# Performance work log

Hardware: AMD Instinct MI355X
Metric: run time of the kernel (lower is better)

Reference implementation:

```python
import jax, jax.numpy as jnp
import numpy as np

B, RULE_DIM, E, P, TOP_K = 8192, 128, 64, 16, 3
EPS = 1e-5
CONF_THRESH = 0.1


def _ln(x, g, b):
    # torch.nn.LayerNorm: biased variance, eps=1e-5
    m = x.mean(-1, keepdims=True)
    v = ((x - m) ** 2).mean(-1, keepdims=True)
    return (x - m) / jnp.sqrt(v + EPS) * g + b


def setup_inputs() -> dict:
    key = jax.random.key(0)
    ks = jax.random.split(key, 8)
    s = lambda fan: 1.0 / np.sqrt(fan)
    return {
        "rule_embedding": jax.random.normal(ks[0], (B, RULE_DIM), jnp.float32),
        "rp_w1": jax.random.normal(ks[1], (RULE_DIM, 256), jnp.float32) * s(RULE_DIM),
        "rp_b1": jnp.zeros((256,), jnp.float32),
        "rp_g1": jnp.ones((256,), jnp.float32),
        "rp_be1": jnp.zeros((256,), jnp.float32),
        "rp_w2": jax.random.normal(ks[2], (256, 512), jnp.float32) * s(256),
        "rp_b2": jnp.zeros((512,), jnp.float32),
        "rp_g2": jnp.ones((512,), jnp.float32),
        "rp_be2": jnp.zeros((512,), jnp.float32),
        "op_w": jax.random.normal(ks[3], (512, E), jnp.float32) * s(512),
        "op_b": jnp.zeros((E,), jnp.float32),
        "pe_w1": jax.random.normal(ks[4], (E, 512, 256), jnp.float32) * s(512),
        "pe_b1": jnp.zeros((E, 256), jnp.float32),
        "pe_g": jnp.ones((E, 256), jnp.float32),
        "pe_beta": jnp.zeros((E, 256), jnp.float32),
        "pe_w2": jax.random.normal(ks[5], (E, 256, P), jnp.float32) * s(256),
        "pe_b2": jnp.zeros((E, P), jnp.float32),
    }


def reference(rule_embedding, rp_w1, rp_b1, rp_g1, rp_be1, rp_w2, rp_b2,
              rp_g2, rp_be2, op_w, op_b, pe_w1, pe_b1, pe_g, pe_beta,
              pe_w2, pe_b2):
    # rule_parser: Linear -> LN -> ReLU -> Linear -> LN -> ReLU
    h = jax.nn.relu(_ln(rule_embedding @ rp_w1 + rp_b1, rp_g1, rp_be1))   # [B,256]
    features = jax.nn.relu(_ln(h @ rp_w2 + rp_b2, rp_g2, rp_be2))         # [B,512]

    # op routing: softmax + top-k
    op_probs = jax.nn.softmax(features @ op_w + op_b, axis=-1)            # [B,E]
    top_probs, top_idx = jax.lax.top_k(op_probs, TOP_K)                   # [B,K]

    # per-op param predictor MLP, evaluated for every expert (vmap over E)
    def expert(w1, b1, g, be, w2, b2):
        z = jax.nn.relu(_ln(features @ w1 + b1, g, be))                   # [B,256]
        return z @ w2 + b2                                                # [B,P]

    h2_all = jax.vmap(expert)(pe_w1, pe_b1, pe_g, pe_beta, pe_w2, pe_b2)  # [E,B,P]

    # gather the selected expert's raw param logits per (token, slot)
    params_sel = h2_all[top_idx, jnp.arange(B)[:, None], :]               # [B,K,P]

    # original skips ops with confidence < 0.1 -> mask them out
    mask = (top_probs >= CONF_THRESH).astype(params_sel.dtype)            # [B,K]
    params_out = params_sel * mask[..., None]

    return top_probs, top_idx, params_out
```

## Files before the change

### kernel.cpp

```cpp
#include <hip/hip_runtime.h>
#include <math.h>

#define Bv   8192
#define EPSv 1e-5f
#define CONFv 0.1f
#define MB (1024*1024)

typedef __attribute__((ext_vector_type(8))) short short8;
typedef __attribute__((ext_vector_type(4))) float f32x4;

__device__ __forceinline__ float wave_sum64(float v){
  #pragma unroll
  for (int o = 32; o; o >>= 1) v += __shfl_xor(v, o, 64);
  return v;
}

__device__ __forceinline__ void split3f(float x, short &h, short &m, short &l){
  unsigned u = __float_as_uint(x);
  h = (short)(u >> 16);
  float r1 = x - __uint_as_float(u & 0xffff0000u);
  unsigned u1 = __float_as_uint(r1);
  m = (short)(u1 >> 16);
  float r2 = r1 - __uint_as_float(u1 & 0xffff0000u);
  l = (short)(__float_as_uint(r2) >> 16);
}

__device__ __forceinline__ void split2f(float x, short &h, short &m){
  unsigned u = __float_as_uint(x);
  h = (short)(u >> 16);
  float r1 = x - __uint_as_float(u & 0xffff0000u);
  m = (short)(__float_as_uint(r1) >> 16);
}

__device__ __forceinline__ f32x4 mfma5(short8 ah, short8 am,
                                       short8 bh, short8 bm, short8 bl, f32x4 c){
  c = __builtin_amdgcn_mfma_f32_16x16x32_bf16(am, bm, c, 0, 0, 0);
  c = __builtin_amdgcn_mfma_f32_16x16x32_bf16(ah, bl, c, 0, 0, 0);
  c = __builtin_amdgcn_mfma_f32_16x16x32_bf16(am, bh, c, 0, 0, 0);
  c = __builtin_amdgcn_mfma_f32_16x16x32_bf16(ah, bm, c, 0, 0, 0);
  c = __builtin_amdgcn_mfma_f32_16x16x32_bf16(ah, bh, c, 0, 0, 0);
  return c;
}

__device__ __forceinline__ f32x4 mfma3(short8 ah, short8 al,
                                       short8 bh, short8 bl, f32x4 c){
  c = __builtin_amdgcn_mfma_f32_16x16x32_bf16(al, bh, c, 0, 0, 0);
  c = __builtin_amdgcn_mfma_f32_16x16x32_bf16(ah, bl, c, 0, 0, 0);
  c = __builtin_amdgcn_mfma_f32_16x16x32_bf16(ah, bh, c, 0, 0, 0);
  return c;
}

__global__ __launch_bounds__(256) void k_pack(const float* __restrict__ pw1,
    const float* __restrict__ pw2, const float* __restrict__ w1,
    const float* __restrict__ w2, const float* __restrict__ opw,
    unsigned short* __restrict__ p1, unsigned short* __restrict__ p2,
    unsigned short* __restrict__ w1p, unsigned short* __restrict__ w2p,
    unsigned short* __restrict__ opwp, int* __restrict__ cnt)
{
  int bid = blockIdx.x;
  if (bid < 4096){
    int t = bid*256 + threadIdx.x;
    int e = t >> 14, rem = t & 16383, kg = rem >> 8, n = rem & 255;
    const float* src = pw1 + ((size_t)e << 17) + (size_t)(kg*8)*256 + n;
    short8 h, l;
    #pragma unroll
    for (int j = 0; j < 8; j++){
      float w = src[(size_t)j*256];
      unsigned u = __float_as_uint(w);
      float r2 = w - __uint_as_float(u & 0xffff0000u);
      h[j] = (short)(u >> 16);
      l[j] = (short)(__float_as_uint(r2) >> 16);
    }
    int idx8 = ((((n >> 4)*16 + (kg >> 2))*64) + (kg & 3)*16 + (n & 15)) << 3;
    unsigned short* ep = p1 + (size_t)e * 262144;
    *(short8*)(ep + idx8)          = h;
    *(short8*)(ep + 131072 + idx8) = l;
  } else if (bid < 4224){
    int t = (bid - 4096)*256 + threadIdx.x;
    int e = t >> 9, rem = t & 511, kg = rem >> 4, n = rem & 15;
    const float* src = pw2 + (size_t)e*4096 + (size_t)(kg*8)*16 + n;
    short8 h, l;
    #pragma unroll
    for (int j = 0; j < 8; j++){
      float w = src[(size_t)j*16];
      unsigned u = __float_as_uint(w);
      float r2 = w - __uint_as_float(u & 0xffff0000u);
      h[j] = (short)(u >> 16);
      l[j] = (short)(__float_as_uint(r2) >> 16);
    }
    int idx8 = (((kg >> 2)*64) + (kg & 3)*16 + n) << 3;
    unsigned short* ep = p2 + (size_t)e * 8192;
    *(short8*)(ep + idx8)        = h;
    *(short8*)(ep + 4096 + idx8) = l;
  } else if (bid < 4352){
    int gid = (bid - 4224)*256 + threadIdx.x;
    int k = gid >> 8, n = gid & 255;
    short h, m, l;
    split3f(w1[gid], h, m, l);
    int idx = (((n >> 4)*4 + (k >> 5))*64 + (((k >> 3) & 3)*16 + (n & 15)))*8 + (k & 7);
    w1p[idx]             = (unsigned short)h;
    w1p[32768 + idx]     = (unsigned short)m;
    w1p[2*32768 + idx]   = (unsigned short)l;
  } else if (bid < 4864){
    int gid = (bid - 4352)*256 + threadIdx.x;
    int k = gid >> 9, n = gid & 511;
    short h, m, l;
    split3f(w2[gid], h, m, l);
    int idx = (((n >> 4)*8 + (k >> 5))*64 + (((k >> 3) & 3)*16 + (n & 15)))*8 + (k & 7);
    w2p[idx]             = (unsigned short)h;
    w2p[131072 + idx]    = (unsigned short)m;
    w2p[2*131072 + idx]  = (unsigned short)l;
  } else if (bid < 4992){
    int gid = (bid - 4864)*256 + threadIdx.x;
    int k = gid >> 6, n = gid & 63;
    short h, m, l;
    split3f(opw[gid], h, m, l);
    int idx = (((n >> 4)*16 + (k >> 5))*64 + (((k >> 3) & 3)*16 + (n & 15)))*8 + (k & 7);
    opwp[idx]            = (unsigned short)h;
    opwp[32768 + idx]    = (unsigned short)m;
    opwp[2*32768 + idx]  = (unsigned short)l;
  } else {
    if (threadIdx.x < 64) cnt[threadIdx.x] = 0;
  }
}

__global__ __launch_bounds__(1024) void k_fused(const float* __restrict__ X,
    const unsigned short* __restrict__ w1p, const float* __restrict__ b1,
    const float* __restrict__ g1, const float* __restrict__ be1,
    const unsigned short* __restrict__ w2p, const float* __restrict__ b2,
    const float* __restrict__ g2, const float* __restrict__ be2,
    const unsigned short* __restrict__ opwp, const float* __restrict__ opb,
    unsigned short* __restrict__ fh, unsigned short* __restrict__ fl,
    float* __restrict__ dout, int* __restrict__ cnt, int* __restrict__ list)
{
  extern __shared__ unsigned char smem[];
  unsigned short* xh  = (unsigned short*)smem;
  unsigned short* xm  = xh + 4096;
  unsigned short* hbh = xh + 8192;
  unsigned short* hbm = xh + 16384;
  unsigned short* gah = xh;
  unsigned short* gam = xh + 16384;
  __shared__ float ps[32][20];
  __shared__ float pq[32][20];
  __shared__ float mi[32][2];
  __shared__ float lg[32][64];

  const int tid = threadIdx.x;
  const int r0  = blockIdx.x * 32;
  const int wave = tid >> 6, lane = tid & 63, lquad = lane >> 4, l15 = lane & 15;

  {
    int r = tid >> 5, c4 = tid & 31;
    float4 v = ((const float4*)X)[(size_t)(r0+r)*32 + c4];
    unsigned u0 = __float_as_uint(v.x), u1 = __float_as_uint(v.y);
    unsigned u2 = __float_as_uint(v.z), u3 = __float_as_uint(v.w);
    float m0 = v.x - __uint_as_float(u0 & 0xffff0000u);
    float m1 = v.y - __uint_as_float(u1 & 0xffff0000u);
    float m2 = v.z - __uint_as_float(u2 & 0xffff0000u);
    float m3 = v.w - __uint_as_float(u3 & 0xffff0000u);
    unsigned hp0 = (u0 >> 16) | (u1 & 0xffff0000u);
    unsigned hp1 = (u2 >> 16) | (u3 & 0xffff0000u);
    unsigned mp0 = (__float_as_uint(m0) >> 16) | (__float_as_uint(m1) & 0xffff0000u);
    unsigned mp1 = (__float_as_uint(m2) >> 16) | (__float_as_uint(m3) & 0xffff0000u);
    int gk = c4 >> 1, half = c4 & 1;
    int off = r*128 + ((gk ^ (r & 7)) << 3) + half*4;
    ((unsigned*)(xh + off))[0] = hp0;
    ((unsigned*)(xh + off))[1] = hp1;
    ((unsigned*)(xm + off))[0] = mp0;
    ((unsigned*)(xm + off))[1] = mp1;
  }
  __syncthreads();

  float bcol1, gcol1, becol1;
  {
    int col = wave*16 + l15;
    bcol1 = b1[col]; gcol1 = g1[col]; becol1 = be1[col];
  }
  {
    f32x4 acc[2];
    acc[0] = (f32x4){0.f,0.f,0.f,0.f};
    acc[1] = (f32x4){0.f,0.f,0.f,0.f};
    const int pstride = 32768;
    for (int ks4 = 0; ks4 < 4; ks4++){
      const unsigned short* bp = w1p + (((wave*4 + ks4)*64 + lane) << 3);
      short8 bh = *(const short8*)bp;
      short8 bm = *(const short8*)(bp + pstride);
      short8 bl = *(const short8*)(bp + 2*pstride);
      #pragma unroll
      for (int mt = 0; mt < 2; mt++){
        int r = mt*16 + l15;
        int off = r*128 + (((ks4*4 + lquad) ^ (r & 7)) << 3);
        short8 ah = *(const short8*)(xh + off);
        short8 am = *(const short8*)(xm + off);
        acc[mt] = mfma5(ah, am, bh, bm, bl, acc[mt]);
      }
    }
    #pragma unroll
    for (int mt = 0; mt < 2; mt++)
      #pragma unroll
      for (int reg = 0; reg < 4; reg++){
        float z = acc[mt][reg] + bcol1;
        float s = z, q = z*z;
        #pragma unroll
        for (int o = 1; o < 16; o <<= 1){ s += __shfl_xor(s, o, 64); q += __shfl_xor(q, o, 64); }
        int row = mt*16 + lquad*4 + reg;
        if (l15 == 0){ ps[row][wave] = s; pq[row][wave] = q; }
      }
    __syncthreads();
    if (tid < 32){
      int row = tid;
      float4 s0 = *(const float4*)&ps[row][0],  s1 = *(const float4*)&ps[row][4];
      float4 s2 = *(const float4*)&ps[row][8],  s3 = *(const float4*)&ps[row][12];
      float4 q0 = *(const float4*)&pq[row][0],  q1 = *(const float4*)&pq[row][4];
      float4 q2 = *(const float4*)&pq[row][8],  q3 = *(const float4*)&pq[row][12];
      float s = s0.x; s += s0.y; s += s0.z; s += s0.w;
      s += s1.x; s += s1.y; s += s1.z; s += s1.w;
      s += s2.x; s += s2.y; s += s2.z; s += s2.w;
      s += s3.x; s += s3.y; s += s3.z; s += s3.w;
      float q = q0.x; q += q0.y; q += q0.z; q += q0.w;
      q += q1.x; q += q1.y; q += q1.z; q += q1.w;
      q += q2.x; q += q2.y; q += q2.z; q += q2.w;
      q += q3.x; q += q3.y; q += q3.z; q += q3.w;
      float mean = s * (1.0f/256.0f);
      float var  = q * (1.0f/256.0f) - mean*mean;
      mi[row][0] = mean;
      mi[row][1] = 1.0f / sqrtf(var + EPSv);
    }
    __syncthreads();
    #pragma unroll
    for (int mt = 0; mt < 2; mt++)
      #pragma unroll
      for (int reg = 0; reg < 4; reg++){
        int row = mt*16 + lquad*4 + reg;
        float2 mv = *(const float2*)mi[row];
        int col = wave*16 + l15;
        float z = acc[mt][reg] + bcol1;
        float y = fmaxf((z - mv.x)*mv.y*gcol1 + becol1, 0.f);
        short hh, mm2;
        split2f(y, hh, mm2);
        int gg = col >> 3, c7 = col & 7;
        int adr = row*256 + ((gg ^ (row & 7)) << 3) + c7;
        hbh[adr] = (unsigned short)hh;
        hbm[adr] = (unsigned short)mm2;
      }
  }
  __syncthreads();

  f32x4 acc2[2][2];
  #pragma unroll
  for (int mt = 0; mt < 2; mt++)
    #pragma unroll
    for (int nt = 0; nt < 2; nt++) acc2[mt][nt] = (f32x4){0.f,0.f,0.f,0.f};
  {
    const int pstride = 131072;
    for (int ks4 = 0; ks4 < 8; ks4++){
      short8 ah[2], am[2];
      #pragma unroll
      for (int mt = 0; mt < 2; mt++){
        int r = mt*16 + l15;
        int off = r*256 + (((ks4*4 + lquad) ^ (r & 7)) << 3);
        ah[mt] = *(const short8*)(hbh + off);
        am[mt] = *(const short8*)(hbm + off);
      }
      #pragma unroll
      for (int nt = 0; nt < 2; nt++){
        int ntg = wave*2 + nt;
        const unsigned short* bp = w2p + (((ntg*8 + ks4)*64 + lane) << 3);
        short8 bh = *(const short8*)bp;
        short8 bm = *(const short8*)(bp + pstride);
        short8 bl = *(const short8*)(bp + 2*pstride);
        #pragma unroll
        for (int mt = 0; mt < 2; mt++)
          acc2[mt][nt] = mfma5(ah[mt], am[mt], bh, bm, bl, acc2[mt][nt]);
      }
    }
  }

  float bcol[2], gcol[2], becol[2];
  #pragma unroll
  for (int nt = 0; nt < 2; nt++){
    int col = (wave*2 + nt)*16 + l15;
    bcol[nt] = b2[col]; gcol[nt] = g2[col]; becol[nt] = be2[col];
  }
  #pragma unroll
  for (int mt = 0; mt < 2; mt++)
    #pragma unroll
    for (int reg = 0; reg < 4; reg++){
      float s = 0.f, q = 0.f;
      #pragma unroll
      for (int nt = 0; nt < 2; nt++){
        float z = acc2[mt][nt][reg] + bcol[nt];
        s += z; q += z*z;
      }
      #pragma unroll
      for (int o = 1; o < 16; o <<= 1){ s += __shfl_xor(s, o, 64); q += __shfl_xor(q, o, 64); }
      int row = mt*16 + lquad*4 + reg;
      if (l15 == 0){ ps[row][wave] = s; pq[row][wave] = q; }
    }
  __syncthreads();
  if (tid < 32){
    int row = tid;
    float4 s0 = *(const float4*)&ps[row][0],  s1 = *(const float4*)&ps[row][4];
    float4 s2 = *(const float4*)&ps[row][8],  s3 = *(const float4*)&ps[row][12];
    float4 q0 = *(const float4*)&pq[row][0],  q1 = *(const float4*)&pq[row][4];
    float4 q2 = *(const float4*)&pq[row][8],  q3 = *(const float4*)&pq[row][12];
    float s = s0.x; s += s0.y; s += s0.z; s += s0.w;
    s += s1.x; s += s1.y; s += s1.z; s += s1.w;
    s += s2.x; s += s2.y; s += s2.z; s += s2.w;
    s += s3.x; s += s3.y; s += s3.z; s += s3.w;
    float q = q0.x; q += q0.y; q += q0.z; q += q0.w;
    q += q1.x; q += q1.y; q += q1.z; q += q1.w;
    q += q2.x; q += q2.y; q += q2.z; q += q2.w;
    q += q3.x; q += q3.y; q += q3.z; q += q3.w;
    float mean = s * (1.0f/512.0f);
    float var  = q * (1.0f/512.0f) - mean*mean;
    mi[row][0] = mean;
    mi[row][1] = 1.0f / sqrtf(var + EPSv);
  }
  __syncthreads();

  #pragma unroll
  for (int mt = 0; mt < 2; mt++)
    #pragma unroll
    for (int reg = 0; reg < 4; reg++){
      int row = mt*16 + lquad*4 + reg;
      float2 mv = *(const float2*)mi[row];
      #pragma unroll
      for (int nt = 0; nt < 2; nt++){
        int col = (wave*2 + nt)*16 + l15;
        float z = acc2[mt][nt][reg] + bcol[nt];
        float y = fmaxf((z - mv.x)*mv.y*gcol[nt] + becol[nt], 0.f);
        short hh, mm2;
        split2f(y, hh, mm2);
        int gg = col >> 3, c7 = col & 7;
        int adr = row*512 + ((gg ^ (row & 7)) << 3) + c7;
        gah[adr] = (unsigned short)hh;
        gam[adr] = (unsigned short)mm2;
      }
    }
  __syncthreads();

  if (wave < 4){
    f32x4 accg[2];
    accg[0] = (f32x4){0.f,0.f,0.f,0.f};
    accg[1] = (f32x4){0.f,0.f,0.f,0.f};
    for (int kt = 0; kt < 16; kt++){
      const unsigned short* bp = opwp + (((wave*16 + kt)*64 + lane) << 3);
      short8 bh = *(const short8*)bp;
      short8 bm = *(const short8*)(bp + 32768);
      short8 bl = *(const short8*)(bp + 65536);
      #pragma unroll
      for (int mt = 0; mt < 2; mt++){
        int r = mt*16 + l15;
        int off = r*512 + (((kt*4 + lquad) ^ (r & 7)) << 3);
        short8 ah = *(const short8*)(gah + off);
        short8 am = *(const short8*)(gam + off);
        accg[mt] = mfma5(ah, am, bh, bm, bl, accg[mt]);
      }
    }
    float opbv = opb[wave*16 + l15];
    #pragma unroll
    for (int mt = 0; mt < 2; mt++)
      #pragma unroll
      for (int reg = 0; reg < 4; reg++)
        lg[mt*16 + lquad*4 + reg][wave*16 + l15] = accg[mt][reg] + opbv;
  } else {
    int t4 = (wave - 4)*64 + lane;
    for (int i = t4; i < 4096; i += 768){
      int p = i >> 11, rem = i & 2047, r = rem >> 6, gg = rem & 63;
      short8 v = *(const short8*)((p ? gam : gah) + r*512 + ((gg ^ (r & 7)) << 3));
      unsigned short* dst = (p ? fl : fh) + (size_t)(r0 + r)*512 + gg*8;
      *(short8*)dst = v;
    }
  }
  __syncthreads();

  {
    for (int rr = 0; rr < 2; rr++){
      int r = wave*2 + rr, row = r0 + r;
      float l = lg[r][lane];
      float mx = l;
      #pragma unroll
      for (int o = 32; o; o >>= 1) mx = fmaxf(mx, __shfl_xor(mx, o, 64));
      float p = expf(l - mx);
      float s = wave_sum64(p);
      p /= s;
      float pv = p;
      for (int j = 0; j < 3; j++){
        float v = pv; int idx = lane;
        #pragma unroll
        for (int o = 32; o; o >>= 1){
          float ov = __shfl_xor(v, o, 64);
          int   oi = __shfl_xor(idx, o, 64);
          if (ov > v || (ov == v && oi < idx)){ v = ov; idx = oi; }
        }
        if (lane == 0){
          dout[(size_t)row*3 + j]                = v;
          dout[(size_t)Bv*3 + (size_t)row*3 + j] = (float)idx;
        }
        if (v >= CONFv){
          if (lane == 0){
            int pos = atomicAdd(&cnt[idx], 1);
            list[idx*Bv + pos] = (row << 2) | j;
          }
        } else {
          if (lane < 16) dout[(size_t)Bv*6 + (size_t)row*48 + j*16 + lane] = 0.f;
        }
        if (lane == idx) pv = -1.0f;
      }
    }
  }
}

__global__ __launch_bounds__(512) void k_expert(const unsigned short* __restrict__ fh,
    const unsigned short* __restrict__ fl,
    const unsigned short* __restrict__ p1, const float* __restrict__ b1,
    const float* __restrict__ g,  const float* __restrict__ beta,
    const unsigned short* __restrict__ p2, const float* __restrict__ b2,
    const int* __restrict__ cnt,  const int* __restrict__ list,
    float* __restrict__ dout)
{
  extern __shared__ unsigned char smem[];
  unsigned short* xh = (unsigned short*)smem;
  unsigned short* xl = xh + 32*512;
  unsigned short* zp = (unsigned short*)smem;
  __shared__ float ps[32][12];
  __shared__ float pq[32][12];
  __shared__ float mi[32][2];
  __shared__ int sdesc[3];

  const int tid = threadIdx.x;
  const int wave = tid >> 6, lane = tid & 63;
  const int lquad = lane >> 4, l15 = lane & 15;

  if (wave == 0){
    int c  = cnt[lane];
    int tl = (c + 31) >> 5;
    int incl = tl;
    #pragma unroll
    for (int o = 1; o < 64; o <<= 1){
      int v = __shfl_up(incl, o, 64);
      if (lane >= o) incl += v;
    }
    int total = __shfl(incl, 63, 64);
    int G   = (total + 7) >> 3;
    int grp = blockIdx.x & 7, rr = blockIdx.x >> 3;
    int lgc = grp*G + rr;
    int ok  = (G > 0) && (rr < G) && (lgc < total);
    unsigned long long bm = __ballot(ok && (incl > lgc));
    if (lane == 0){
      if (!ok || bm == 0ull){ sdesc[0] = -1; }
      else {
        int e = __ffsll((long long)bm) - 1;
        sdesc[0] = e; sdesc[1] = lgc; sdesc[2] = 0;
      }
    }
    if (bm != 0ull && ok){
      int e = __ffsll((long long)bm) - 1;
      int excl = __shfl(incl - tl, e, 64);
      int ne   = __shfl(c, e, 64);
      if (lane == 0){ sdesc[1] = lgc - excl; sdesc[2] = ne; }
    }
  }
  __syncthreads();
  const int e = sdesc[0];
  if (e < 0) return;
  const int t = sdesc[1];
  const int n = sdesc[2];
  const int base = t * 32;
  const int m = min(32, n - base);
  const int* lrow = list + e*Bv + base;

  for (int i = tid; i < 4096; i += 512){
    int p = i >> 11, rem = i & 2047, r = rem >> 6, gg = rem & 63;
    int ev = lrow[(r < m) ? r : 0];
    int row = ev >> 2;
    const unsigned short* src = (p ? fl : fh) + (size_t)row*512 + gg*8;
    short8 v = *(const short8*)src;
    unsigned short* dst = (p ? xl : xh) + r*512 + ((gg ^ (r & 7)) << 3);
    *(short8*)dst = v;
  }
  __syncthreads();

  const unsigned short* p1e = p1 + (size_t)e * 262144;
  f32x4 acc[2][2];
  #pragma unroll
  for (int mt = 0; mt < 2; mt++)
    #pragma unroll
    for (int nt = 0; nt < 2; nt++) acc[mt][nt] = (f32x4){0.f,0.f,0.f,0.f};

  for (int kt = 0; kt < 16; kt++){
    short8 ah[2], al[2];
    int gk = kt*4 + lquad;
    #pragma unroll
    for (int mt = 0; mt < 2; mt++){
      int r = mt*16 + l15;
      int off = r*512 + ((gk ^ (r & 7)) << 3);
      ah[mt] = *(const short8*)(xh + off);
      al[mt] = *(const short8*)(xl + off);
    }
    #pragma unroll
    for (int nt = 0; nt < 2; nt++){
      int ntg = wave*2 + nt;
      const unsigned short* bp = p1e + (((ntg*16 + kt)*64 + lane) << 3);
      short8 bh = *(const short8*)bp;
      short8 bl = *(const short8*)(bp + 131072);
      #pragma unroll
      for (int mt = 0; mt < 2; mt++)
        acc[mt][nt] = mfma3(ah[mt], al[mt], bh, bl, acc[mt][nt]);
    }
  }

  float bb[2], gv[2], bv[2];
  #pragma unroll
  for (int nt = 0; nt < 2; nt++){
    int col = (wave*2 + nt)*16 + l15;
    bb[nt] = b1[e*256 + col];
    gv[nt] = g[e*256 + col];
    bv[nt] = beta[e*256 + col];
  }
  #pragma unroll
  for (int mt = 0; mt < 2; mt++)
    #pragma unroll
    for (int reg = 0; reg < 4; reg++){
      float s = 0.f, q = 0.f;
      #pragma unroll
      for (int nt = 0; nt < 2; nt++){
        float z = acc[mt][nt][reg] + bb[nt];
        s += z; q += z*z;
      }
      #pragma unroll
      for (int o = 1; o < 16; o <<= 1){ s += __shfl_xor(s, o, 64); q += __shfl_xor(q, o, 64); }
      int row = mt*16 + lquad*4 + reg;
      if (l15 == 0){ ps[row][wave] = s; pq[row][wave] = q; }
    }
  __syncthreads();
  if (tid < 32){
    int row = tid;
    float4 s0 = *(const float4*)&ps[row][0], s1 = *(const float4*)&ps[row][4];
    float4 q0 = *(const float4*)&pq[row][0], q1 = *(const float4*)&pq[row][4];
    float s = s0.x; s += s0.y; s += s0.z; s += s0.w;
    s += s1.x; s += s1.y; s += s1.z; s += s1.w;
    float q = q0.x; q += q0.y; q += q0.z; q += q0.w;
    q += q1.x; q += q1.y; q += q1.z; q += q1.w;
    float mean = s * (1.0f/256.0f);
    float var  = q * (1.0f/256.0f) - mean*mean;
    mi[row][0] = mean;
    mi[row][1] = 1.0f / sqrtf(var + EPSv);
  }
  __syncthreads();

  #pragma unroll
  for (int mt = 0; mt < 2; mt++)
    #pragma unroll
    for (int reg = 0; reg < 4; reg++){
      int row = mt*16 + lquad*4 + reg;
      float2 mv = *(const float2*)mi[row];
      #pragma unroll
      for (int nt = 0; nt < 2; nt++){
        int col = (wave*2 + nt)*16 + l15;
        float z = acc[mt][nt][reg] + bb[nt];
        float y = fmaxf((z - mv.x)*mv.y*gv[nt] + bv[nt], 0.f);
        short hh, mm2;
        split2f(y, hh, mm2);
        zp[row*528 + col]       = (unsigned short)hh;
        zp[row*528 + 264 + col] = (unsigned short)mm2;
      }
    }
  __syncthreads();

  if (wave < 2){
    const unsigned short* p2e = p2 + (size_t)e * 8192;
    f32x4 acc2 = (f32x4){0.f,0.f,0.f,0.f};
    for (int kt2 = 0; kt2 < 8; kt2++){
      const unsigned short* zb = zp + (wave*16 + l15)*528 + kt2*32 + lquad*8;
      short8 ahh = *(const short8*)zb;
      short8 all2 = *(const short8*)(zb + 264);
      const unsigned short* bp = p2e + ((kt2*64 + lane) << 3);
      short8 bh = *(const short8*)bp;
      short8 bl = *(const short8*)(bp + 4096);
      acc2 = mfma3(ahh, all2, bh, bl, acc2);
    }
    float b2v = b2[e*16 + l15];
    #pragma unroll
    for (int reg = 0; reg < 4; reg++){
      int rl = wave*16 + lquad*4 + reg;
      if (rl < m){
        int ev = lrow[rl];
        int row = ev >> 2, j = ev & 3;
        dout[(size_t)Bv*6 + (size_t)row*48 + j*16 + l15] = acc2[reg] + b2v;
      }
    }
  }
}

extern "C" void kernel_launch(void* const* d_in, const int* in_sizes, int n_in,
                              void* d_out, int out_size, void* d_ws, size_t ws_size,
                              hipStream_t stream)
{
  const float* X   = (const float*)d_in[0];
  const float* w1  = (const float*)d_in[1];
  const float* b1  = (const float*)d_in[2];
  const float* g1  = (const float*)d_in[3];
  const float* be1 = (const float*)d_in[4];
  const float* w2  = (const float*)d_in[5];
  const float* b2  = (const float*)d_in[6];
  const float* g2  = (const float*)d_in[7];
  const float* be2 = (const float*)d_in[8];
  const float* opw = (const float*)d_in[9];
  const float* opb = (const float*)d_in[10];
  const float* pw1 = (const float*)d_in[11];
  const float* pb1 = (const float*)d_in[12];
  const float* pg  = (const float*)d_in[13];
  const float* pbe = (const float*)d_in[14];
  const float* pw2 = (const float*)d_in[15];
  const float* pb2 = (const float*)d_in[16];
  float* out = (float*)d_out;
  char*  ws  = (char*)d_ws;

  unsigned short* p1E    = (unsigned short*)ws;
  unsigned short* p2E    = (unsigned short*)(ws + (size_t)32*MB);
  unsigned short* w1p_rp = (unsigned short*)(ws + (size_t)33*MB);
  unsigned short* w2p_rp = (unsigned short*)(ws + (size_t)34*MB);
  unsigned short* opwp   = (unsigned short*)(ws + (size_t)35*MB);
  unsigned short* fh     = (unsigned short*)(ws + (size_t)36*MB);
  unsigned short* fl     = (unsigned short*)(ws + (size_t)44*MB);
  int*            list   = (int*)(ws + (size_t)52*MB);
  int*            cnt    = (int*)(ws + (size_t)54*MB);

  k_pack  <<<4993, 256, 0, stream>>>(pw1, pw2, w1, w2, opw, p1E, p2E,
                                     w1p_rp, w2p_rp, opwp, cnt);
  k_fused <<<256, 1024, 65536, stream>>>(X, w1p_rp, b1, g1, be1,
                                         w2p_rp, b2, g2, be2, opwp, opb,
                                         fh, fl, out, cnt, list);
  k_expert<<<832,  512, 65536, stream>>>(fh, fl, p1E, pb1, pg, pbe, p2E, pb2,
                                         cnt, list, out);
}
```

Before: 172.4 us.

## Move expert weight packing into rule-parser kernel to overlap with compute

The large per-expert weight split/pack work (pe_w1, pe_w2 to bf16 hi/lo) is removed from the pre-pack kernel and appended as extra blocks of the fused rule-parser kernel. Those extra blocks run alongside the 256 compute blocks, so the 32MB of expert weight conversion can overlap with the rule-parser and routing work instead of running serially before it. The small pre-pack kernel now converts only the rule-parser and routing weights. The packing blocks still request 64KB dynamic shared memory per 1024-thread block, which may limit how many of them co-reside with the compute blocks.

```diff
diff --git a/kernel.cpp b/kernel.cpp
--- a/kernel.cpp
+++ b/kernel.cpp
@@ -50,50 +50,15 @@
   return c;
 }
 
-__global__ __launch_bounds__(256) void k_pack(const float* __restrict__ pw1,
-    const float* __restrict__ pw2, const float* __restrict__ w1,
-    const float* __restrict__ w2, const float* __restrict__ opw,
-    unsigned short* __restrict__ p1, unsigned short* __restrict__ p2,
+__global__ __launch_bounds__(256) void k_pre(
+    const float* __restrict__ w1, const float* __restrict__ w2,
+    const float* __restrict__ opw,
     unsigned short* __restrict__ w1p, unsigned short* __restrict__ w2p,
     unsigned short* __restrict__ opwp, int* __restrict__ cnt)
 {
   int bid = blockIdx.x;
-  if (bid < 4096){
-    int t = bid*256 + threadIdx.x;
-    int e = t >> 14, rem = t & 16383, kg = rem >> 8, n = rem & 255;
-    const float* src = pw1 + ((size_t)e << 17) + (size_t)(kg*8)*256 + n;
-    short8 h, l;
-    #pragma unroll
-    for (int j = 0; j < 8; j++){
-      float w = src[(size_t)j*256];
-      unsigned u = __float_as_uint(w);
-      float r2 = w - __uint_as_float(u & 0xffff0000u);
-      h[j] = (short)(u >> 16);
-      l[j] = (short)(__float_as_uint(r2) >> 16);
-    }
-    int idx8 = ((((n >> 4)*16 + (kg >> 2))*64) + (kg & 3)*16 + (n & 15)) << 3;
-    unsigned short* ep = p1 + (size_t)e * 262144;
-    *(short8*)(ep + idx8)          = h;
-    *(short8*)(ep + 131072 + idx8) = l;
-  } else if (bid < 4224){
-    int t = (bid - 4096)*256 + threadIdx.x;
-    int e = t >> 9, rem = t & 511, kg = rem >> 4, n = rem & 15;
-    const float* src = pw2 + (size_t)e*4096 + (size_t)(kg*8)*16 + n;
-    short8 h, l;
-    #pragma unroll
-    for (int j = 0; j < 8; j++){
-      float w = src[(size_t)j*16];
-      unsigned u = __float_as_uint(w);
-      float r2 = w - __uint_as_float(u & 0xffff0000u);
-      h[j] = (short)(u >> 16);
-      l[j] = (short)(__float_as_uint(r2) >> 16);
-    }
-    int idx8 = (((kg >> 2)*64) + (kg & 3)*16 + n) << 3;
-    unsigned short* ep = p2 + (size_t)e * 8192;
-    *(short8*)(ep + idx8)        = h;
-    *(short8*)(ep + 4096 + idx8) = l;
-  } else if (bid < 4352){
-    int gid = (bid - 4224)*256 + threadIdx.x;
+  if (bid < 128){
+    int gid = bid*256 + threadIdx.x;
     int k = gid >> 8, n = gid & 255;
     short h, m, l;
     split3f(w1[gid], h, m, l);
@@ -101,8 +66,8 @@
     w1p[idx]             = (unsigned short)h;
     w1p[32768 + idx]     = (unsigned short)m;
     w1p[2*32768 + idx]   = (unsigned short)l;
-  } else if (bid < 4864){
-    int gid = (bid - 4352)*256 + threadIdx.x;
+  } else if (bid < 640){
+    int gid = (bid - 128)*256 + threadIdx.x;
     int k = gid >> 9, n = gid & 511;
     short h, m, l;
     split3f(w2[gid], h, m, l);
@@ -110,8 +75,8 @@
     w2p[idx]             = (unsigned short)h;
     w2p[131072 + idx]    = (unsigned short)m;
     w2p[2*131072 + idx]  = (unsigned short)l;
-  } else if (bid < 4992){
-    int gid = (bid - 4864)*256 + threadIdx.x;
+  } else if (bid < 768){
+    int gid = (bid - 640)*256 + threadIdx.x;
     int k = gid >> 6, n = gid & 63;
     short h, m, l;
     split3f(opw[gid], h, m, l);
@@ -131,9 +96,52 @@
     const float* __restrict__ g2, const float* __restrict__ be2,
     const unsigned short* __restrict__ opwp, const float* __restrict__ opb,
     unsigned short* __restrict__ fh, unsigned short* __restrict__ fl,
-    float* __restrict__ dout, int* __restrict__ cnt, int* __restrict__ list)
+    float* __restrict__ dout, int* __restrict__ cnt, int* __restrict__ list,
+    const float* __restrict__ pw1, const float* __restrict__ pw2,
+    unsigned short* __restrict__ p1, unsigned short* __restrict__ p2)
 {
   extern __shared__ unsigned char smem[];
+
+  if (blockIdx.x >= 256){
+    int pb = blockIdx.x - 256;
+    if (pb < 1024){
+      int t = pb*1024 + threadIdx.x;
+      int e = t >> 14, rem = t & 16383, kg = rem >> 8, n = rem & 255;
+      const float* src = pw1 + ((size_t)e << 17) + (size_t)(kg*8)*256 + n;
+      short8 h, l;
+      #pragma unroll
+      for (int j = 0; j < 8; j++){
+        float w = src[(size_t)j*256];
+        unsigned u = __float_as_uint(w);
+        float r2 = w - __uint_as_float(u & 0xffff0000u);
+        h[j] = (short)(u >> 16);
+        l[j] = (short)(__float_as_uint(r2) >> 16);
+      }
+      int idx8 = ((((n >> 4)*16 + (kg >> 2))*64) + (kg & 3)*16 + (n & 15)) << 3;
+      unsigned short* ep = p1 + (size_t)e * 262144;
+      *(short8*)(ep + idx8)          = h;
+      *(short8*)(ep + 131072 + idx8) = l;
+    } else {
+      int t = (pb - 1024)*1024 + threadIdx.x;
+      int e = t >> 9, rem = t & 511, kg = rem >> 4, n = rem & 15;
+      const float* src = pw2 + (size_t)e*4096 + (size_t)(kg*8)*16 + n;
+      short8 h, l;
+      #pragma unroll
+      for (int j = 0; j < 8; j++){
+        float w = src[(size_t)j*16];
+        unsigned u = __float_as_uint(w);
+        float r2 = w - __uint_as_float(u & 0xffff0000u);
+        h[j] = (short)(u >> 16);
+        l[j] = (short)(__float_as_uint(r2) >> 16);
+      }
+      int idx8 = (((kg >> 2)*64) + (kg & 3)*16 + n) << 3;
+      unsigned short* ep = p2 + (size_t)e * 8192;
+      *(short8*)(ep + idx8)        = h;
+      *(short8*)(ep + 4096 + idx8) = l;
+    }
+    return;
+  }
+
   unsigned short* xh  = (unsigned short*)smem;
   unsigned short* xm  = xh + 4096;
   unsigned short* hbh = xh + 8192;
@@ -628,11 +636,11 @@
   int*            list   = (int*)(ws + (size_t)52*MB);
   int*            cnt    = (int*)(ws + (size_t)54*MB);
 
-  k_pack  <<<4993, 256, 0, stream>>>(pw1, pw2, w1, w2, opw, p1E, p2E,
-                                     w1p_rp, w2p_rp, opwp, cnt);
-  k_fused <<<256, 1024, 65536, stream>>>(X, w1p_rp, b1, g1, be1,
-                                         w2p_rp, b2, g2, be2, opwp, opb,
-                                         fh, fl, out, cnt, list);
+  k_pre   <<<769, 256, 0, stream>>>(w1, w2, opw, w1p_rp, w2p_rp, opwp, cnt);
+  k_fused <<<1312, 1024, 65536, stream>>>(X, w1p_rp, b1, g1, be1,
+                                          w2p_rp, b2, g2, be2, opwp, opb,
+                                          fh, fl, out, cnt, list,
+                                          pw1, pw2, p1E, p2E);
   k_expert<<<832,  512, 65536, stream>>>(fh, fl, p1E, pb1, pg, pbe, p2E, pb2,
                                          cnt, list, out);
 }
```

Result: no change. 169.9 us (-1.5%).
